# Kernel tuning notes

Hardware: AMD Instinct MI355X
Metric: run time of the kernel (lower is better)

Reference implementation:

```python
import jax, jax.numpy as jnp
import numpy as np

EPSILON = 1e-06
PATCH_SIZE = 16


def _patches(x, ps):
    # im2col-style patch extraction matching the torch loop order:
    # patches are ordered row-major over (i, j) patch grid, pixels flattened row-major.
    b, c, h, w = x.shape
    hp, wp = h // ps, w // ps  # H,W chosen as multiples of ps -> no reflection padding
    x = x.reshape(b, c, hp, ps, wp, ps)
    x = x.transpose(0, 1, 2, 4, 3, 5)  # (b, c, hp, wp, ps, ps)
    return x.reshape(b, c, hp * wp, ps * ps), (hp, wp)


def setup_inputs() -> dict:
    key = jax.random.key(0)
    k0, k1, k2 = jax.random.split(key, 3)
    shape = (16, 3, 512, 512)
    return {
        "out": jax.random.normal(k0, shape, dtype=jnp.float32),
        "x1": jax.random.normal(k1, shape, dtype=jnp.float32),
        "x2": jax.random.normal(k2, shape, dtype=jnp.float32),
    }


def reference(out, x1, x2):
    ps = PATCH_SIZE
    b, c, h, w = out.shape
    patch0, _ = _patches(out, ps)   # (b, c, n, p)
    patch1, (hp, wp) = _patches(x1, ps)
    patch2, _ = _patches(x2, ps)
    p = ps * ps

    mu1 = jnp.mean(patch1, axis=3, keepdims=True)  # (b,c,n,1)
    # NOTE: original code (faithfully reproduced) uses mu1 for sd2 as well
    # (mu2_re = mu1.view(...)), so sd2 is computed around mu1.
    sd1 = jnp.sqrt(jnp.sum((patch1 - mu1) ** 2, axis=3) / p)  # (b,c,n)
    sd2 = jnp.sqrt(jnp.sum((patch2 - mu1) ** 2, axis=3) / p)  # (b,c,n)

    denom = sd1 + sd2 + EPSILON
    w1 = (sd1 / denom)[..., None]  # (b,c,n,1)
    w2 = (sd2 / denom)[..., None]

    H2, W2 = hp * ps, wp * ps
    w1_img = jnp.broadcast_to(w1, (b, c, hp * wp, p)).reshape(b, c, H2, W2)
    w2_img = jnp.broadcast_to(w2, (b, c, hp * wp, p)).reshape(b, c, H2, W2)

    loss = jnp.mean((patch0 - (w1 * patch1 + w2 * patch2)) ** 2)
    return (loss, w1_img, w2_img)
```

## Files before the change

kernel.cpp:

```cpp
#include <hip/hip_runtime.h>

constexpr int IMG         = 512;
constexpr int PLANES      = 48;
constexpr int NPATCH      = 1024;
constexpr int TOTAL_PATCH = PLANES * NPATCH;
constexpr int PLANE_ELEMS = IMG * IMG;
constexpr long long TOTAL_ELEMS = (long long)PLANES * PLANE_ELEMS;
constexpr float  EPS = 1e-6f;

__device__ __forceinline__ float waveReduceSum(float v) {
#pragma unroll
    for (int m = 1; m < 64; m <<= 1)
        v += __shfl_xor(v, m, 64);
    return v;
}

__global__ __launch_bounds__(256) void patch_main(
    const float* __restrict__ p0,
    const float* __restrict__ p1,
    const float* __restrict__ p2,
    float* __restrict__ dout,
    float* __restrict__ partial)
{
    const int lane  = threadIdx.x & 63;
    const int wv    = threadIdx.x >> 6;
    const int patch = blockIdx.x * 4 + wv;
    const int plane = patch >> 10;
    const int n     = patch & 1023;
    const int pi    = n >> 5;
    const int pj    = n & 31;

    const int r  = lane >> 2;
    const int c4 = (lane & 3) << 2;

    const size_t ibase = (size_t)plane * PLANE_ELEMS
                       + (size_t)(pi * 16 + r) * IMG
                       + (size_t)(pj * 16 + c4);

    const float4 a = *(const float4*)(p0 + ibase);
    const float4 b = *(const float4*)(p1 + ibase);
    const float4 c = *(const float4*)(p2 + ibase);

    float s = (b.x + b.y) + (b.z + b.w);
    s = waveReduceSum(s);
    const float mu = s * (1.0f / 256.0f);

    float bx = b.x - mu, by = b.y - mu, bz = b.z - mu, bw = b.w - mu;
    float cx = c.x - mu, cy = c.y - mu, cz = c.z - mu, cw = c.w - mu;
    float d1 = (bx*bx + by*by) + (bz*bz + bw*bw);
    float d2 = (cx*cx + cy*cy) + (cz*cz + cw*cw);
    d1 = waveReduceSum(d1);
    d2 = waveReduceSum(d2);

    const float sd1 = sqrtf(d1 * (1.0f / 256.0f));
    const float sd2 = sqrtf(d2 * (1.0f / 256.0f));
    const float denom = sd1 + sd2 + EPS;
    const float w1 = sd1 / denom;
    const float w2 = sd2 / denom;

    float e0 = a.x - (w1 * b.x + w2 * c.x);
    float e1 = a.y - (w1 * b.y + w2 * c.y);
    float e2 = a.z - (w1 * b.z + w2 * c.z);
    float e3 = a.w - (w1 * b.w + w2 * c.w);
    float l = (e0*e0 + e1*e1) + (e2*e2 + e3*e3);
    l = waveReduceSum(l);

    float* __restrict__ w1o = dout + 1;
    float* __restrict__ w2o = dout + 1 + TOTAL_ELEMS;
    const size_t ob = (size_t)plane * PLANE_ELEMS + (size_t)n * 256 + (size_t)lane * 4;
#pragma unroll
    for (int k = 0; k < 4; ++k) w1o[ob + k] = w1;
#pragma unroll
    for (int k = 0; k < 4; ++k) w2o[ob + k] = w2;

    __shared__ float ls[4];
    if (lane == 0) ls[wv] = l;
    __syncthreads();
    if (threadIdx.x == 0)
        partial[blockIdx.x] = (ls[0] + ls[1]) + (ls[2] + ls[3]);
}

__global__ __launch_bounds__(256) void patch_reduce(
    const float* __restrict__ partial, float* __restrict__ dout)
{
    constexpr int NPART = TOTAL_PATCH / 4;
    double s = 0.0;
    for (int i = threadIdx.x; i < NPART; i += 256)
        s += (double)partial[i];
#pragma unroll
    for (int m = 1; m < 64; m <<= 1)
        s += __shfl_xor(s, m, 64);
    __shared__ double sm[4];
    if ((threadIdx.x & 63) == 0) sm[threadIdx.x >> 6] = s;
    __syncthreads();
    if (threadIdx.x == 0)
        dout[0] = (float)(((sm[0] + sm[1]) + (sm[2] + sm[3])) / (double)TOTAL_ELEMS);
}

extern "C" void kernel_launch(void* const* d_in, const int* in_sizes, int n_in,
                              void* d_out, int out_size, void* d_ws, size_t ws_size,
                              hipStream_t stream) {
    const float* p0 = (const float*)d_in[0];
    const float* p1 = (const float*)d_in[1];
    const float* p2 = (const float*)d_in[2];
    float* dout    = (float*)d_out;
    float* partial = (float*)d_ws;

    patch_main<<<TOTAL_PATCH / 4, 256, 0, stream>>>(p0, p1, p2, dout, partial);
    patch_reduce<<<1, 256, 0, stream>>>(partial, dout);
}
```

Before: 55.08 us.

## Process two patches per wave with DPP reductions and aligned float4 weight stores

Each wave now handles two patches, so twice as many independent loads are in flight and the grid has half as many blocks. The shuffle-based wave reductions become DPP row operations followed by a readlane of lane 63. The weight-image writes, which start at dout+1 and so sit one float off 16-byte alignment, become aligned float4 stores at offset 3 plus four scalar edge stores, replacing eight scalar stores per lane. The cost is more registers per thread and more complex store indexing.

```diff
diff --git a/kernel.cpp b/kernel.cpp
--- a/kernel.cpp
+++ b/kernel.cpp
@@ -2,79 +2,107 @@
 
 constexpr int IMG         = 512;
 constexpr int PLANES      = 48;
-constexpr int NPATCH      = 1024;
-constexpr int TOTAL_PATCH = PLANES * NPATCH;
+constexpr int TOTAL_PATCH = PLANES * 1024;
 constexpr int PLANE_ELEMS = IMG * IMG;
 constexpr long long TOTAL_ELEMS = (long long)PLANES * PLANE_ELEMS;
 constexpr float  EPS = 1e-6f;
+constexpr int PATCHES_PER_BLOCK = 8;
+constexpr int NBLOCKS = TOTAL_PATCH / PATCHES_PER_BLOCK;
 
-__device__ __forceinline__ float waveReduceSum(float v) {
-#pragma unroll
-    for (int m = 1; m < 64; m <<= 1)
-        v += __shfl_xor(v, m, 64);
+template <int CTRL, int ROW_MASK>
+__device__ __forceinline__ float dpp_add(float v) {
+    int x = __builtin_amdgcn_update_dpp(0, __float_as_int(v), CTRL, ROW_MASK, 0xF, false);
+    return v + __int_as_float(x);
+}
+__device__ __forceinline__ float wave_total63(float v) {
+    v = dpp_add<0x111, 0xF>(v);
+    v = dpp_add<0x112, 0xF>(v);
+    v = dpp_add<0x114, 0xF>(v);
+    v = dpp_add<0x118, 0xF>(v);
+    v = dpp_add<0x142, 0xA>(v);
+    v = dpp_add<0x143, 0xC>(v);
     return v;
 }
+__device__ __forceinline__ float wave_allsum(float v) {
+    v = wave_total63(v);
+    return __int_as_float(__builtin_amdgcn_readlane(__float_as_int(v), 63));
+}
 
-__global__ __launch_bounds__(256) void patch_main(
-    const float* __restrict__ p0,
-    const float* __restrict__ p1,
-    const float* __restrict__ p2,
-    float* __restrict__ dout,
-    float* __restrict__ partial)
-{
-    const int lane  = threadIdx.x & 63;
-    const int wv    = threadIdx.x >> 6;
-    const int patch = blockIdx.x * 4 + wv;
+__device__ __forceinline__ size_t in_base(int patch, int lane) {
     const int plane = patch >> 10;
     const int n     = patch & 1023;
-    const int pi    = n >> 5;
-    const int pj    = n & 31;
+    const int pi    = n >> 5, pj = n & 31;
+    const int r     = lane >> 2, c4 = (lane & 3) << 2;
+    return (size_t)plane * PLANE_ELEMS + (size_t)(pi * 16 + r) * IMG + (size_t)(pj * 16 + c4);
+}
 
-    const int r  = lane >> 2;
-    const int c4 = (lane & 3) << 2;
-
-    const size_t ibase = (size_t)plane * PLANE_ELEMS
-                       + (size_t)(pi * 16 + r) * IMG
-                       + (size_t)(pj * 16 + c4);
-
-    const float4 a = *(const float4*)(p0 + ibase);
-    const float4 b = *(const float4*)(p1 + ibase);
-    const float4 c = *(const float4*)(p2 + ibase);
-
-    float s = (b.x + b.y) + (b.z + b.w);
-    s = waveReduceSum(s);
-    const float mu = s * (1.0f / 256.0f);
+__device__ __forceinline__ void process_patch(const float4& a, const float4& b, const float4& c,
+                                              float& w1, float& w2, float& loss63) {
+    float s  = (b.x + b.y) + (b.z + b.w);
+    const float mu = wave_allsum(s) * (1.0f / 256.0f);
 
     float bx = b.x - mu, by = b.y - mu, bz = b.z - mu, bw = b.w - mu;
     float cx = c.x - mu, cy = c.y - mu, cz = c.z - mu, cw = c.w - mu;
     float d1 = (bx*bx + by*by) + (bz*bz + bw*bw);
     float d2 = (cx*cx + cy*cy) + (cz*cz + cw*cw);
-    d1 = waveReduceSum(d1);
-    d2 = waveReduceSum(d2);
+    d1 = wave_allsum(d1);
+    d2 = wave_allsum(d2);
 
     const float sd1 = sqrtf(d1 * (1.0f / 256.0f));
     const float sd2 = sqrtf(d2 * (1.0f / 256.0f));
     const float denom = sd1 + sd2 + EPS;
-    const float w1 = sd1 / denom;
-    const float w2 = sd2 / denom;
+    w1 = sd1 / denom;
+    w2 = sd2 / denom;
 
     float e0 = a.x - (w1 * b.x + w2 * c.x);
     float e1 = a.y - (w1 * b.y + w2 * c.y);
     float e2 = a.z - (w1 * b.z + w2 * c.z);
     float e3 = a.w - (w1 * b.w + w2 * c.w);
-    float l = (e0*e0 + e1*e1) + (e2*e2 + e3*e3);
-    l = waveReduceSum(l);
+    loss63 = wave_total63((e0*e0 + e1*e1) + (e2*e2 + e3*e3));
+}
+
+__device__ __forceinline__ void store_w(float* __restrict__ base, float w, int lane) {
+    if (lane < 63) {
+        float4 v = make_float4(w, w, w, w);
+        *(float4*)(base + 3 + (lane << 2)) = v;
+    }
+    if (lane < 4) base[lane == 3 ? 255 : lane] = w;
+}
+
+__global__ __launch_bounds__(256) void patch_main(
+    const float* __restrict__ p0, const float* __restrict__ p1, const float* __restrict__ p2,
+    float* __restrict__ dout, float* __restrict__ partial)
+{
+    const int lane = threadIdx.x & 63;
+    const int wv   = threadIdx.x >> 6;
+    const int pA   = blockIdx.x * PATCHES_PER_BLOCK + wv * 2;
+    const int pB   = pA + 1;
+
+    const size_t iA = in_base(pA, lane);
+    const size_t iB = in_base(pB, lane);
+
+    const float4 aA = *(const float4*)(p0 + iA);
+    const float4 bA = *(const float4*)(p1 + iA);
+    const float4 cA = *(const float4*)(p2 + iA);
+    const float4 aB = *(const float4*)(p0 + iB);
+    const float4 bB = *(const float4*)(p1 + iB);
+    const float4 cB = *(const float4*)(p2 + iB);
+
+    float w1A, w2A, lA, w1B, w2B, lB;
+    process_patch(aA, bA, cA, w1A, w2A, lA);
+    process_patch(aB, bB, cB, w1B, w2B, lB);
 
     float* __restrict__ w1o = dout + 1;
     float* __restrict__ w2o = dout + 1 + TOTAL_ELEMS;
-    const size_t ob = (size_t)plane * PLANE_ELEMS + (size_t)n * 256 + (size_t)lane * 4;
-#pragma unroll
-    for (int k = 0; k < 4; ++k) w1o[ob + k] = w1;
-#pragma unroll
-    for (int k = 0; k < 4; ++k) w2o[ob + k] = w2;
+    const size_t obA = ((size_t)(pA >> 10)) * PLANE_ELEMS + (size_t)(pA & 1023) * 256;
+    const size_t obB = ((size_t)(pB >> 10)) * PLANE_ELEMS + (size_t)(pB & 1023) * 256;
+    store_w(w1o + obA, w1A, lane);
+    store_w(w2o + obA, w2A, lane);
+    store_w(w1o + obB, w1B, lane);
+    store_w(w2o + obB, w2B, lane);
 
     __shared__ float ls[4];
-    if (lane == 0) ls[wv] = l;
+    if (lane == 63) ls[wv] = lA + lB;
     __syncthreads();
     if (threadIdx.x == 0)
         partial[blockIdx.x] = (ls[0] + ls[1]) + (ls[2] + ls[3]);
@@ -83,7 +111,7 @@
 __global__ __launch_bounds__(256) void patch_reduce(
     const float* __restrict__ partial, float* __restrict__ dout)
 {
-    constexpr int NPART = TOTAL_PATCH / 4;
+    constexpr int NPART = NBLOCKS;
     double s = 0.0;
     for (int i = threadIdx.x; i < NPART; i += 256)
         s += (double)partial[i];
@@ -106,6 +134,6 @@
     float* dout    = (float*)d_out;
     float* partial = (float*)d_ws;
 
-    patch_main<<<TOTAL_PATCH / 4, 256, 0, stream>>>(p0, p1, p2, dout, partial);
+    patch_main<<<NBLOCKS, 256, 0, stream>>>(p0, p1, p2, dout, partial);
     patch_reduce<<<1, 256, 0, stream>>>(partial, dout);
 }
```

Result: faster. 50.50 us (-8.3%).

## Process four patches per wave using moment sums and a single-pass atomic loss reduction

Applied to the files above, without the earlier changes.

Each wave now covers four horizontally adjacent patches. Each lane loads full 64-byte row segments, so reads are more coalesced. The variance and the loss are computed from first and second moments (S, Q, cross products) reduced with DPP, swizzle and permlane, which removes the per-element second pass. The separate reduce kernel is replaced by a double atomic accumulator with a last-block counter, plus a memset. Weight stores are shifted by three floats to account for the offset-by-one output base. The moment form of the loss risks cancellation error, and it adds atomics and a memset launch.

```diff
diff --git a/kernel.cpp b/kernel.cpp
--- a/kernel.cpp
+++ b/kernel.cpp
@@ -1,100 +1,130 @@
 #include <hip/hip_runtime.h>
 
 constexpr int IMG         = 512;
-constexpr int PLANES      = 48;
-constexpr int NPATCH      = 1024;
-constexpr int TOTAL_PATCH = PLANES * NPATCH;
 constexpr int PLANE_ELEMS = IMG * IMG;
-constexpr long long TOTAL_ELEMS = (long long)PLANES * PLANE_ELEMS;
+constexpr int TOTAL_PATCH = 48 * 1024;
+constexpr long long TOTAL_ELEMS = 12582912LL;
 constexpr float  EPS = 1e-6f;
+constexpr int NBLOCKS = TOTAL_PATCH / 16;
 
-__device__ __forceinline__ float waveReduceSum(float v) {
-#pragma unroll
-    for (int m = 1; m < 64; m <<= 1)
-        v += __shfl_xor(v, m, 64);
-    return v;
+template <int CTRL>
+__device__ __forceinline__ float dpp_add(float v) {
+    int x = __builtin_amdgcn_update_dpp(0, __float_as_int(v), CTRL, 0xF, 0xF, false);
+    return v + __int_as_float(x);
+}
+
+__device__ __forceinline__ float seg_reduce(float v) {
+    v = dpp_add<0xB1>(v);
+    v = dpp_add<0x4E>(v);
+    v += __int_as_float(__builtin_amdgcn_ds_swizzle(__float_as_int(v), 0x401F));
+    auto p = __builtin_amdgcn_permlane32_swap(__float_as_int(v), __float_as_int(v), false, false);
+    return __int_as_float(p[0]) + __int_as_float(p[1]);
+}
+
+__device__ __forceinline__ float read_lane_f(float v, int l) {
+    return __int_as_float(__builtin_amdgcn_readlane(__float_as_int(v), l));
+}
+
+__device__ __forceinline__ void store_w(float* __restrict__ base, float w, int lane) {
+    if (lane < 63) {
+        float4 v = make_float4(w, w, w, w);
+        *(float4*)(base + 3 + (lane << 2)) = v;
+    }
+    if (lane < 4) base[lane == 3 ? 255 : lane] = w;
 }
 
 __global__ __launch_bounds__(256) void patch_main(
-    const float* __restrict__ p0,
-    const float* __restrict__ p1,
-    const float* __restrict__ p2,
-    float* __restrict__ dout,
-    float* __restrict__ partial)
+    const float* __restrict__ p0, const float* __restrict__ p1, const float* __restrict__ p2,
+    float* __restrict__ dout, double* __restrict__ acc, unsigned* __restrict__ cnt)
 {
     const int lane  = threadIdx.x & 63;
     const int wv    = threadIdx.x >> 6;
-    const int patch = blockIdx.x * 4 + wv;
-    const int plane = patch >> 10;
-    const int n     = patch & 1023;
-    const int pi    = n >> 5;
-    const int pj    = n & 31;
+    const int wgid  = blockIdx.x * 4 + wv;
+    const int pbase = wgid * 4;
+    const int plane = pbase >> 10;
+    const int nb    = pbase & 1023;
+    const int pi    = nb >> 5;
+    const int pjb   = nb & 31;
 
-    const int r  = lane >> 2;
-    const int c4 = (lane & 3) << 2;
+    const int colgrp = lane & 15;
+    const int rowin  = lane >> 4;
+    const size_t base = (size_t)plane * PLANE_ELEMS
+                      + (size_t)(pi * 16 + rowin) * IMG
+                      + (size_t)(pjb * 16 + colgrp * 4);
 
-    const size_t ibase = (size_t)plane * PLANE_ELEMS
-                       + (size_t)(pi * 16 + r) * IMG
-                       + (size_t)(pj * 16 + c4);
+    float4 a[4], b[4], c[4];
+#pragma unroll
+    for (int i = 0; i < 4; ++i) {
+        const size_t off = base + (size_t)(4 * i) * IMG;
+        a[i] = *(const float4*)(p0 + off);
+        b[i] = *(const float4*)(p1 + off);
+        c[i] = *(const float4*)(p2 + off);
+    }
 
-    const float4 a = *(const float4*)(p0 + ibase);
-    const float4 b = *(const float4*)(p1 + ibase);
-    const float4 c = *(const float4*)(p2 + ibase);
+    float S1 = 0, S2 = 0, Q0 = 0, Q1 = 0, Q2 = 0, P01 = 0, P02 = 0, P12 = 0;
+#pragma unroll
+    for (int i = 0; i < 4; ++i) {
+        const float av[4] = {a[i].x, a[i].y, a[i].z, a[i].w};
+        const float bv[4] = {b[i].x, b[i].y, b[i].z, b[i].w};
+        const float cv[4] = {c[i].x, c[i].y, c[i].z, c[i].w};
+#pragma unroll
+        for (int j = 0; j < 4; ++j) {
+            S1 += bv[j];               S2 += cv[j];
+            Q0  = fmaf(av[j], av[j], Q0);
+            Q1  = fmaf(bv[j], bv[j], Q1);
+            Q2  = fmaf(cv[j], cv[j], Q2);
+            P01 = fmaf(av[j], bv[j], P01);
+            P02 = fmaf(av[j], cv[j], P02);
+            P12 = fmaf(bv[j], cv[j], P12);
+        }
+    }
 
-    float s = (b.x + b.y) + (b.z + b.w);
-    s = waveReduceSum(s);
-    const float mu = s * (1.0f / 256.0f);
+    S1 = seg_reduce(S1);  S2 = seg_reduce(S2);
+    Q0 = seg_reduce(Q0);  Q1 = seg_reduce(Q1);  Q2 = seg_reduce(Q2);
+    P01 = seg_reduce(P01); P02 = seg_reduce(P02); P12 = seg_reduce(P12);
 
-    float bx = b.x - mu, by = b.y - mu, bz = b.z - mu, bw = b.w - mu;
-    float cx = c.x - mu, cy = c.y - mu, cz = c.z - mu, cw = c.w - mu;
-    float d1 = (bx*bx + by*by) + (bz*bz + bw*bw);
-    float d2 = (cx*cx + cy*cy) + (cz*cz + cw*cw);
-    d1 = waveReduceSum(d1);
-    d2 = waveReduceSum(d2);
-
+    const float mu = S1 * (1.0f / 256.0f);
+    const float d1 = fmaxf(Q1 - mu * S1, 0.0f);
+    const float d2 = fmaxf(Q2 - 2.0f * mu * S2 + mu * S1, 0.0f);
     const float sd1 = sqrtf(d1 * (1.0f / 256.0f));
     const float sd2 = sqrtf(d2 * (1.0f / 256.0f));
     const float denom = sd1 + sd2 + EPS;
     const float w1 = sd1 / denom;
     const float w2 = sd2 / denom;
+    const float L  = Q0 + w1 * w1 * Q1 + w2 * w2 * Q2
+                   - 2.0f * (w1 * P01 + w2 * P02 - w1 * w2 * P12);
 
-    float e0 = a.x - (w1 * b.x + w2 * c.x);
-    float e1 = a.y - (w1 * b.y + w2 * c.y);
-    float e2 = a.z - (w1 * b.z + w2 * c.z);
-    float e3 = a.w - (w1 * b.w + w2 * c.w);
-    float l = (e0*e0 + e1*e1) + (e2*e2 + e3*e3);
-    l = waveReduceSum(l);
+    float w1q[4], w2q[4];
+#pragma unroll
+    for (int q = 0; q < 4; ++q) {
+        w1q[q] = read_lane_f(w1, 4 * q);
+        w2q[q] = read_lane_f(w2, 4 * q);
+    }
+    const float wl = (read_lane_f(L, 0) + read_lane_f(L, 4))
+                   + (read_lane_f(L, 8) + read_lane_f(L, 12));
 
     float* __restrict__ w1o = dout + 1;
     float* __restrict__ w2o = dout + 1 + TOTAL_ELEMS;
-    const size_t ob = (size_t)plane * PLANE_ELEMS + (size_t)n * 256 + (size_t)lane * 4;
+    const size_t wb = (size_t)plane * PLANE_ELEMS + (size_t)nb * 256;
 #pragma unroll
-    for (int k = 0; k < 4; ++k) w1o[ob + k] = w1;
-#pragma unroll
-    for (int k = 0; k < 4; ++k) w2o[ob + k] = w2;
+    for (int q = 0; q < 4; ++q) {
+        store_w(w1o + wb + q * 256, w1q[q], lane);
+        store_w(w2o + wb + q * 256, w2q[q], lane);
+    }
 
     __shared__ float ls[4];
-    if (lane == 0) ls[wv] = l;
+    if (lane == 0) ls[wv] = wl;
     __syncthreads();
-    if (threadIdx.x == 0)
-        partial[blockIdx.x] = (ls[0] + ls[1]) + (ls[2] + ls[3]);
-}
-
-__global__ __launch_bounds__(256) void patch_reduce(
-    const float* __restrict__ partial, float* __restrict__ dout)
-{
-    constexpr int NPART = TOTAL_PATCH / 4;
-    double s = 0.0;
-    for (int i = threadIdx.x; i < NPART; i += 256)
-        s += (double)partial[i];
-#pragma unroll
-    for (int m = 1; m < 64; m <<= 1)
-        s += __shfl_xor(s, m, 64);
-    __shared__ double sm[4];
-    if ((threadIdx.x & 63) == 0) sm[threadIdx.x >> 6] = s;
-    __syncthreads();
-    if (threadIdx.x == 0)
-        dout[0] = (float)(((sm[0] + sm[1]) + (sm[2] + sm[3])) / (double)TOTAL_ELEMS);
+    if (threadIdx.x == 0) {
+        const float bl = (ls[0] + ls[1]) + (ls[2] + ls[3]);
+        atomicAdd(acc, (double)bl);
+        __threadfence();
+        const unsigned old = atomicAdd(cnt, 1u);
+        if (old == (unsigned)(NBLOCKS - 1)) {
+            const double total = atomicAdd(acc, 0.0);
+            dout[0] = (float)(total / (double)TOTAL_ELEMS);
+        }
+    }
 }
 
 extern "C" void kernel_launch(void* const* d_in, const int* in_sizes, int n_in,
@@ -103,9 +133,10 @@
     const float* p0 = (const float*)d_in[0];
     const float* p1 = (const float*)d_in[1];
     const float* p2 = (const float*)d_in[2];
-    float* dout    = (float*)d_out;
-    float* partial = (float*)d_ws;
+    float* dout = (float*)d_out;
+    double* acc = (double*)d_ws;
+    unsigned* cnt = (unsigned*)((char*)d_ws + 8);
 
-    patch_main<<<TOTAL_PATCH / 4, 256, 0, stream>>>(p0, p1, p2, dout, partial);
-    patch_reduce<<<1, 256, 0, stream>>>(partial, dout);
+    (void)hipMemsetAsync(d_ws, 0, 16, stream);
+    patch_main<<<NBLOCKS, 256, 0, stream>>>(p0, p1, p2, dout, acc, cnt);
 }
```

After: 165.9 us. +201.2%, slower.
